# Kernel optimization log

Hardware: AMD Instinct MI355X
Metric: run time of the kernel (lower is better)

Reference implementation:

```python
import jax, jax.numpy as jnp
import numpy as np

B, A, S, C = 32, 3, 52, 80


def setup_inputs() -> dict:
    key = jax.random.key(0)
    k1, k2, k3, k4 = jax.random.split(key, 4)
    predictions = jax.random.normal(k1, (B, A, S, S, 5 + C), dtype=jnp.float32)
    # target: [obj in {0,1}, x, y, w, h, class]
    obj = (jax.random.uniform(k2, (B, A, S, S, 1)) < 0.05).astype(jnp.float32)
    boxes = jax.random.uniform(k3, (B, A, S, S, 4), dtype=jnp.float32)
    cls = jax.random.randint(k4, (B, A, S, S, 1), 0, C).astype(jnp.float32)
    target = jnp.concatenate([obj, boxes, cls], axis=-1)
    return {"predictions": predictions, "target": target}


def _iou_midpoint(b1, b2):
    # b1, b2: [..., 4] in (cx, cy, w, h) midpoint format
    b1x1 = b1[..., 0] - b1[..., 2] / 2
    b1y1 = b1[..., 1] - b1[..., 3] / 2
    b1x2 = b1[..., 0] + b1[..., 2] / 2
    b1y2 = b1[..., 1] + b1[..., 3] / 2
    b2x1 = b2[..., 0] - b2[..., 2] / 2
    b2y1 = b2[..., 1] - b2[..., 3] / 2
    b2x2 = b2[..., 0] + b2[..., 2] / 2
    b2y2 = b2[..., 1] + b2[..., 3] / 2
    x1 = jnp.maximum(b1x1, b2x1)
    y1 = jnp.maximum(b1y1, b2y1)
    x2 = jnp.minimum(b1x2, b2x2)
    y2 = jnp.minimum(b1y2, b2y2)
    inter = jnp.clip(x2 - x1, 0) * jnp.clip(y2 - y1, 0)
    a1 = jnp.abs((b1x2 - b1x1) * (b1y2 - b1y1))
    a2 = jnp.abs((b2x2 - b2x1) * (b2y2 - b2y1))
    return inter / (a1 + a2 - inter + 1e-6)


def _masked_mean(x, mask, denom):
    return jnp.sum(jnp.where(mask, x, 0.0)) / jnp.maximum(denom, 1.0)


def reference(predictions, target):
    LAMBDA_CLASS, LAMBDA_NOOBJ, LAMBDA_OBJ, LAMBDA_BOX = 1.0, 0.5, 1.0, 5.0
    tobj = target[..., 0]
    obj = tobj == 1.0        # [B,A,S,S]
    noobj = tobj == 0.0
    n_obj = jnp.sum(obj.astype(jnp.float32))
    n_noobj = jnp.sum(noobj.astype(jnp.float32))

    # --- no-object BCEWithLogits (mean over noobj cells, feature dim = 1) ---
    x = predictions[..., 0]
    bce = jnp.maximum(x, 0.0) - x * tobj + jnp.log1p(jnp.exp(-jnp.abs(x)))
    no_object_loss = _masked_mean(bce, noobj, n_noobj)

    # --- object MSE: sigmoid(pred_obj) vs iou * target_obj ---
    # NB: this repo passes raw predictions (cols 0:4) into IoU.
    ious = _iou_midpoint(predictions[..., 0:4], target[..., 1:5])  # [B,A,S,S]
    ious = jax.lax.stop_gradient(ious)
    p_obj = jax.nn.sigmoid(x)
    object_loss = _masked_mean((p_obj - ious * tobj) ** 2, obj, n_obj)

    # --- box MSE: sigmoid(pred[1:5]) vs target[1:5], mean over N*4 elems ---
    sp = jax.nn.sigmoid(predictions[..., 1:5])
    box_se = jnp.sum((sp - target[..., 1:5]) ** 2, axis=-1)  # [B,A,S,S]
    box_loss = jnp.sum(jnp.where(obj, box_se, 0.0)) / jnp.maximum(n_obj * 4.0, 1.0)

    # --- class cross-entropy over obj cells ---
    logits = predictions[..., 5:]
    labels = target[..., 5].astype(jnp.int32)
    logp = jax.nn.log_softmax(logits, axis=-1)
    nll = -jnp.take_along_axis(logp, labels[..., None], axis=-1)[..., 0]
    class_loss = _masked_mean(nll, obj, n_obj)

    return (LAMBDA_BOX * box_loss, LAMBDA_OBJ * object_loss,
            LAMBDA_NOOBJ * no_object_loss, LAMBDA_CLASS * class_loss)
```

## Files before the change

kernel.cpp:

```cpp
#include <hip/hip_runtime.h>
#include <math.h>
#include <stdint.h>

constexpr int NCELL = 32 * 3 * 52 * 52;
constexpr int PS = 85;
constexpr int TPB = 256;
constexpr int NBLK = NCELL / TPB;


__global__ __launch_bounds__(TPB) void yolo_main(const float* __restrict__ pred,
                                                 const float* __restrict__ tgt,
                                                 float* __restrict__ part)
{
    const int tid  = threadIdx.x;
    const int wid  = tid >> 6;
    const int lane = tid & 63;
    const int cell = blockIdx.x * TPB + tid;

    __shared__ float red[4][6];

    const int pi = (cell * PS) >> 2;
    const float4* pa = (const float4*)pred;
    float4 A = pa[pi];
    const int o = cell & 3;
    float p0 = o==0 ? A.x : o==1 ? A.y : o==2 ? A.z : A.w;

    const int ti = (cell * 6) >> 2;
    const float4* pt = (const float4*)tgt;
    float4 TA = pt[ti];
    const bool oh = (cell & 1);
    float t0 = oh ? TA.z : TA.x;

    const bool obj   = (t0 == 1.0f);
    const bool noobj = (t0 == 0.0f);

    float s0=0.f, s1=0.f, s2=0.f, s3=0.f, s4=0.f, s5=0.f;
    float t5 = 0.0f;

    float bce = fmaxf(p0, 0.0f) - p0 * t0 + log1pf(__expf(-fabsf(p0)));
    if (noobj) { s0 = bce; s1 = 1.0f; }

    if (obj) {
        float4 Bv = pa[pi + 1];
        float4 TB = pt[ti + 1];

        float p1 = o==0 ? A.y  : o==1 ? A.z  : o==2 ? A.w  : Bv.x;
        float p2 = o==0 ? A.z  : o==1 ? A.w  : o==2 ? Bv.x : Bv.y;
        float p3 = o==0 ? A.w  : o==1 ? Bv.x : o==2 ? Bv.y : Bv.z;
        float p4 = o==0 ? Bv.x : o==1 ? Bv.y : o==2 ? Bv.z : Bv.w;

        float t1 = oh ? TA.w : TA.y;
        float t2 = oh ? TB.x : TA.z;
        float t3 = oh ? TB.y : TA.w;
        float t4 = oh ? TB.z : TB.x;
        t5       = oh ? TB.w : TB.y;

        float b1x1 = p0 - p2 * 0.5f, b1y1 = p1 - p3 * 0.5f;
        float b1x2 = p0 + p2 * 0.5f, b1y2 = p1 + p3 * 0.5f;
        float b2x1 = t1 - t3 * 0.5f, b2y1 = t2 - t4 * 0.5f;
        float b2x2 = t1 + t3 * 0.5f, b2y2 = t2 + t4 * 0.5f;
        float xi1 = fmaxf(b1x1, b2x1), yi1 = fmaxf(b1y1, b2y1);
        float xi2 = fminf(b1x2, b2x2), yi2 = fminf(b1y2, b2y2);
        float inter = fmaxf(xi2 - xi1, 0.0f) * fmaxf(yi2 - yi1, 0.0f);
        float a1 = fabsf((b1x2 - b1x1) * (b1y2 - b1y1));
        float a2 = fabsf((b2x2 - b2x1) * (b2y2 - b2y1));
        float iou = inter / (a1 + a2 - inter + 1e-6f);

        float pobj = 1.0f / (1.0f + __expf(-p0));
        float dob  = pobj - iou;

        float d1 = 1.0f / (1.0f + __expf(-p1)) - t1;
        float d2 = 1.0f / (1.0f + __expf(-p2)) - t2;
        float d3 = 1.0f / (1.0f + __expf(-p3)) - t3;
        float d4 = 1.0f / (1.0f + __expf(-p4)) - t4;

        s2 = dob * dob;
        s4 = d1*d1 + d2*d2 + d3*d3 + d4*d4;
    }

    unsigned long long mask = __ballot(obj);
    if (lane == 0) s3 = (float)__popcll(mask);

    const int waveCell0 = blockIdx.x * TPB + wid * 64;
    while (mask) {
        int L = __builtin_ctzll(mask);
        mask &= mask - 1;

        const float* row = pred + (size_t)(waveCell0 + L) * PS;
        float v0 = row[5 + lane];
        float v1 = (lane < 16) ? row[69 + lane] : -INFINITY;

        float m = fmaxf(v0, v1);
        #pragma unroll
        for (int off = 1; off < 64; off <<= 1)
            m = fmaxf(m, __shfl_xor(m, off));

        float e = __expf(v0 - m) + ((lane < 16) ? __expf(v1 - m) : 0.0f);
        #pragma unroll
        for (int off = 1; off < 64; off <<= 1)
            e += __shfl_xor(e, off);

        int lbl = (int)__shfl(t5, L);
        float sel = (lbl < 64) ? __shfl(v0, lbl) : __shfl(v1, lbl - 64);

        if (lane == 0) s5 += __logf(e) - (sel - m);
    }

    #pragma unroll
    for (int off = 1; off < 64; off <<= 1) {
        s0 += __shfl_xor(s0, off);
        s1 += __shfl_xor(s1, off);
        s2 += __shfl_xor(s2, off);
        s3 += __shfl_xor(s3, off);
        s4 += __shfl_xor(s4, off);
        s5 += __shfl_xor(s5, off);
    }

    if (lane == 0) {
        red[wid][0] = s0; red[wid][1] = s1; red[wid][2] = s2;
        red[wid][3] = s3; red[wid][4] = s4; red[wid][5] = s5;
    }
    __syncthreads();
    if (tid == 0) {
        float a0=0.f,a1=0.f,a2=0.f,a3=0.f,a4=0.f,a5=0.f;
        #pragma unroll
        for (int w = 0; w < 4; ++w) {
            a0 += red[w][0]; a1 += red[w][1]; a2 += red[w][2];
            a3 += red[w][3]; a4 += red[w][4]; a5 += red[w][5];
        }
        float4* slot = (float4*)(part + (size_t)blockIdx.x * 8);
        slot[0] = make_float4(a0, a1, a2, a3);
        slot[1] = make_float4(a4, a5, 0.0f, 0.0f);
    }
}

__global__ __launch_bounds__(1024) void yolo_reduce(const float* __restrict__ part,
                                                    float* __restrict__ out)
{
    float a0=0.f,a1=0.f,a2=0.f,a3=0.f,a4=0.f,a5=0.f;
    int i = threadIdx.x;
    if (i < NBLK) {
        const float4* slot = (const float4*)(part + (size_t)i * 8);
        float4 v0 = slot[0];
        float4 v1 = slot[1];
        a0 = v0.x; a1 = v0.y; a2 = v0.z; a3 = v0.w; a4 = v1.x; a5 = v1.y;
    }

    #pragma unroll
    for (int off = 32; off > 0; off >>= 1) {
        a0 += __shfl_down(a0, off);
        a1 += __shfl_down(a1, off);
        a2 += __shfl_down(a2, off);
        a3 += __shfl_down(a3, off);
        a4 += __shfl_down(a4, off);
        a5 += __shfl_down(a5, off);
    }

    __shared__ float red[16][6];
    int lane = threadIdx.x & 63;
    int wid  = threadIdx.x >> 6;
    if (lane == 0) {
        red[wid][0] = a0; red[wid][1] = a1; red[wid][2] = a2;
        red[wid][3] = a3; red[wid][4] = a4; red[wid][5] = a5;
    }
    __syncthreads();
    if (threadIdx.x == 0) {
        float b0=0.f,b1=0.f,b2=0.f,b3=0.f,b4=0.f,b5=0.f;
        #pragma unroll
        for (int w = 0; w < 16; ++w) {
            b0 += red[w][0]; b1 += red[w][1]; b2 += red[w][2];
            b3 += red[w][3]; b4 += red[w][4]; b5 += red[w][5];
        }
        float n_noobj = b1;
        float n_obj   = b3;
        out[0] = 5.0f * b4 / fmaxf(n_obj * 4.0f, 1.0f);
        out[1] = 1.0f * b2 / fmaxf(n_obj, 1.0f);
        out[2] = 0.5f * b0 / fmaxf(n_noobj, 1.0f);
        out[3] = 1.0f * b5 / fmaxf(n_obj, 1.0f);
    }
}

extern "C" void kernel_launch(void* const* d_in, const int* in_sizes, int n_in,
                              void* d_out, int out_size, void* d_ws, size_t ws_size,
                              hipStream_t stream)
{
    const float* pred = (const float*)d_in[0];
    const float* tgt  = (const float*)d_in[1];
    float* out  = (float*)d_out;
    float* part = (float*)d_ws;

    yolo_main<<<NBLK, TPB, 0, stream>>>(pred, tgt, part);
    yolo_reduce<<<1, 1024, 0, stream>>>(part, out);
}
```

Before: 23.57 us.

## Balance per-object softmax work across waves via shared queue with prefetch

Object cells are compacted into a block-wide shared-memory queue, and the four waves take entries round-robin. Before, each wave handled only its own object cells, so a wave with many objects set the block's time. The loop also prefetches the next row's logits to overlap load latency with the current reduction. The cost is two extra __syncthreads and shared memory for the queue.

```diff
diff --git a/kernel.cpp b/kernel.cpp
--- a/kernel.cpp
+++ b/kernel.cpp
@@ -16,8 +16,11 @@
     const int wid  = tid >> 6;
     const int lane = tid & 63;
     const int cell = blockIdx.x * TPB + tid;
+    const int cell0 = blockIdx.x * TPB;
 
     __shared__ float red[4][6];
+    __shared__ int   cnt[4];
+    __shared__ int   qd[TPB];
 
     const int pi = (cell * PS) >> 2;
     const float4* pa = (const float4*)pred;
@@ -35,7 +38,7 @@
     const bool noobj = (t0 == 0.0f);
 
     float s0=0.f, s1=0.f, s2=0.f, s3=0.f, s4=0.f, s5=0.f;
-    float t5 = 0.0f;
+    int lbl_self = 0;
 
     float bce = fmaxf(p0, 0.0f) - p0 * t0 + log1pf(__expf(-fabsf(p0)));
     if (noobj) { s0 = bce; s1 = 1.0f; }
@@ -53,7 +56,8 @@
         float t2 = oh ? TB.x : TA.z;
         float t3 = oh ? TB.y : TA.w;
         float t4 = oh ? TB.z : TB.x;
-        t5       = oh ? TB.w : TB.y;
+        float t5 = oh ? TB.w : TB.y;
+        lbl_self = (int)t5;
 
         float b1x1 = p0 - p2 * 0.5f, b1y1 = p1 - p3 * 0.5f;
         float b1x2 = p0 + p2 * 0.5f, b1y2 = p1 + p3 * 0.5f;
@@ -79,31 +83,58 @@
     }
 
     unsigned long long mask = __ballot(obj);
-    if (lane == 0) s3 = (float)__popcll(mask);
-
-    const int waveCell0 = blockIdx.x * TPB + wid * 64;
-    while (mask) {
-        int L = __builtin_ctzll(mask);
-        mask &= mask - 1;
-
-        const float* row = pred + (size_t)(waveCell0 + L) * PS;
-        float v0 = row[5 + lane];
-        float v1 = (lane < 16) ? row[69 + lane] : -INFINITY;
-
-        float m = fmaxf(v0, v1);
-        #pragma unroll
-        for (int off = 1; off < 64; off <<= 1)
-            m = fmaxf(m, __shfl_xor(m, off));
-
-        float e = __expf(v0 - m) + ((lane < 16) ? __expf(v1 - m) : 0.0f);
-        #pragma unroll
-        for (int off = 1; off < 64; off <<= 1)
-            e += __shfl_xor(e, off);
-
-        int lbl = (int)__shfl(t5, L);
-        float sel = (lbl < 64) ? __shfl(v0, lbl) : __shfl(v1, lbl - 64);
-
-        if (lane == 0) s5 += __logf(e) - (sel - m);
+    int mycnt = __popcll(mask);
+    if (lane == 0) { s3 = (float)mycnt; cnt[wid] = mycnt; }
+    __syncthreads();
+    int qoff = 0;
+    #pragma unroll
+    for (int w = 0; w < 4; ++w) if (w < wid) qoff += cnt[w];
+    const int nq = cnt[0] + cnt[1] + cnt[2] + cnt[3];
+    if (obj) {
+        int rank = __popcll(mask & ((1ull << lane) - 1ull));
+        qd[qoff + rank] = tid | (lbl_self << 8);
+    }
+    __syncthreads();
+
+    {
+        int q = wid;
+        float v0 = -INFINITY, v1 = -INFINITY;
+        int lbl = 0;
+        if (q < nq) {
+            int e = qd[q];
+            const float* row = pred + (size_t)(cell0 + (e & 255)) * PS;
+            lbl = e >> 8;
+            v0 = row[5 + lane];
+            v1 = (lane < 16) ? row[69 + lane] : -INFINITY;
+        }
+        while (q < nq) {
+            int qn = q + 4;
+            float nv0 = -INFINITY, nv1 = -INFINITY;
+            int nlbl = 0;
+            if (qn < nq) {
+                int e = qd[qn];
+                const float* row = pred + (size_t)(cell0 + (e & 255)) * PS;
+                nlbl = e >> 8;
+                nv0 = row[5 + lane];
+                nv1 = (lane < 16) ? row[69 + lane] : -INFINITY;
+            }
+
+            float m = fmaxf(v0, v1);
+            #pragma unroll
+            for (int off = 1; off < 64; off <<= 1)
+                m = fmaxf(m, __shfl_xor(m, off));
+
+            float e = __expf(v0 - m) + ((lane < 16) ? __expf(v1 - m) : 0.0f);
+            #pragma unroll
+            for (int off = 1; off < 64; off <<= 1)
+                e += __shfl_xor(e, off);
+
+            float sel = (lbl < 64) ? __shfl(v0, lbl) : __shfl(v1, lbl - 64);
+            if (lane == 0) s5 += __logf(e) - (sel - m);
+
+            v0 = nv0; v1 = nv1; lbl = nlbl;
+            q = qn;
+        }
     }
 
     #pragma unroll
```

Result: faster. 21.36 us, median of 2 (-9.4%).
